# Kernel optimization log

Measured on AMD Instinct MI355X. Metric: run time of the kernel, lower is better.

The kernel has to match this reference:

```python
import jax, jax.numpy as jnp
import numpy as np
from jax import lax

EPS = 1e-5

def _dsconv(x, dw, pw, g, b, m, v, relu):
    # x: [B,C,H,W]; dw: [C,1,3,3] depthwise; pw: [C,C,1,1] pointwise; eval-mode BN
    C = x.shape[1]
    y = lax.conv_general_dilated(x, dw, (1, 1), 'SAME', feature_group_count=C)
    y = lax.conv_general_dilated(y, pw, (1, 1), 'SAME')
    scale = (g * lax.rsqrt(v + EPS))[None, :, None, None]
    y = y * scale + (b - m * g * lax.rsqrt(v + EPS))[None, :, None, None]
    return jnp.maximum(y, 0.0) if relu else y

def _attention(x, wq, bq, wk, bk, wv, bv, gamma):
    b, c, h, w = x.shape
    n = h * w
    xf = x.reshape(b, c, n)                      # [B,C,N]
    q = jnp.einsum('oc,bcn->bon', wq, xf) + bq[None, :, None]   # [B,C/8,N]
    k = jnp.einsum('oc,bcn->bon', wk, xf) + bk[None, :, None]   # [B,C/8,N]
    v = jnp.einsum('oc,bcn->bon', wv, xf) + bv[None, :, None]   # [B,C,N]
    logits = jnp.einsum('bdm,bdn->bmn', q, k)    # q^T k, [B,N,N]
    attn = jax.nn.softmax(logits, axis=2)
    out = jnp.einsum('bcn,bmn->bcm', v, attn).reshape(b, c, h, w)
    return gamma[0] * out + x

def setup_inputs() -> dict:
    key = jax.random.key(0)
    ks = jax.random.split(key, 20)
    B, C, H, W = 64, 256, 32, 32
    C8 = C // 8
    rn = lambda k, s, sc: (jax.random.normal(k, s, dtype=jnp.float32) * sc)
    return {
        'x': rn(ks[0], (B, C, H, W), 1.0),
        'dw1': rn(ks[1], (C, 1, 3, 3), 0.2),
        'pw1': rn(ks[2], (C, C, 1, 1), 0.06),
        'bn1_g': jax.random.uniform(ks[3], (C,), jnp.float32, 0.5, 1.5),
        'bn1_b': rn(ks[4], (C,), 0.1),
        'bn1_m': rn(ks[5], (C,), 0.1),
        'bn1_v': jax.random.uniform(ks[6], (C,), jnp.float32, 0.5, 1.5),
        'dw2': rn(ks[7], (C, 1, 3, 3), 0.2),
        'pw2': rn(ks[8], (C, C, 1, 1), 0.06),
        'bn2_g': jax.random.uniform(ks[9], (C,), jnp.float32, 0.5, 1.5),
        'bn2_b': rn(ks[10], (C,), 0.1),
        'bn2_m': rn(ks[11], (C,), 0.1),
        'bn2_v': jax.random.uniform(ks[12], (C,), jnp.float32, 0.5, 1.5),
        'wq': rn(ks[13], (C8, C), 0.06),
        'bq': rn(ks[14], (C8,), 0.02),
        'wk': rn(ks[15], (C8, C), 0.06),
        'bk': rn(ks[16], (C8,), 0.02),
        'wv': rn(ks[17], (C, C), 0.06),
        'bv': rn(ks[18], (C,), 0.02),
        'gamma': rn(ks[19], (1,), 0.5),
    }

def reference(x, dw1, pw1, bn1_g, bn1_b, bn1_m, bn1_v,
              dw2, pw2, bn2_g, bn2_b, bn2_m, bn2_v,
              wq, bq, wk, bk, wv, bv, gamma):
    out = _dsconv(x, dw1, pw1, bn1_g, bn1_b, bn1_m, bn1_v, relu=True)
    out = _dsconv(out, dw2, pw2, bn2_g, bn2_b, bn2_m, bn2_v, relu=False)
    out = _attention(out + x, wq, bq, wk, bk, wv, bv, gamma)
    return jnp.maximum(out, 0.0)
```

## Files before the change

### kernel.cpp

```cpp
#include <hip/hip_runtime.h>
#include <cstdint>
#include <cstddef>

#define B_ 64
#define C_ 256
#define N_ 1024
#define LOG2E 1.4426950408889634f

typedef short v8s __attribute__((ext_vector_type(8)));
typedef float v4f __attribute__((ext_vector_type(4)));
typedef unsigned int u32;
typedef unsigned short u16;

#define VMCNT(N) asm volatile("s_waitcnt vmcnt(" #N ")" ::: "memory")
#define LGKM0 asm volatile("s_waitcnt lgkmcnt(0)" ::: "memory")
#define SBAR __builtin_amdgcn_s_barrier()
#define SCHEDB __builtin_amdgcn_sched_barrier(0)

__device__ __forceinline__ float bf2f(u16 u) {
  return __uint_as_float(((u32)u) << 16);
}
__device__ __forceinline__ u16 f2bf(float f) {
  u32 x = __float_as_uint(f);
  x += 0x7fffu + ((x >> 16) & 1u);
  return (u16)(x >> 16);
}
__device__ __forceinline__ u32 pack2(float a, float b) {
  return (u32)f2bf(a) | ((u32)f2bf(b) << 16);
}
__device__ __forceinline__ u32 cvtpk(float lo, float hi) {
  u32 r;
  asm("v_cvt_pk_bf16_f32 %0, %1, %2" : "=v"(r) : "v"(lo), "v"(hi));
  return r;
}

typedef __attribute__((address_space(3))) unsigned int lds_as_t;
typedef __attribute__((address_space(1))) const unsigned int glb_as_t;
__device__ __forceinline__ void ld_lds16(const u16* g, u16* l) {
  __builtin_amdgcn_global_load_lds((glb_as_t*)g, (lds_as_t*)l, 16, 0, 0);
}

__global__ __launch_bounds__(256) void prep(
    const float* __restrict__ g1, const float* __restrict__ b1,
    const float* __restrict__ m1, const float* __restrict__ v1,
    const float* __restrict__ g2, const float* __restrict__ b2,
    const float* __restrict__ m2, const float* __restrict__ v2,
    const float* __restrict__ wq, const float* __restrict__ bq,
    const float* __restrict__ wk, const float* __restrict__ bk,
    const float* __restrict__ wv, const float* __restrict__ bv,
    const float* __restrict__ pw1, const float* __restrict__ pw2,
    const float* __restrict__ dw1, const float* __restrict__ dw2,
    float* __restrict__ scale1, float* __restrict__ shift1,
    float* __restrict__ scale2, float* __restrict__ shift2,
    float* __restrict__ dwT1, float* __restrict__ dwT2,
    u16* __restrict__ pw1b, u16* __restrict__ pw2b, u16* __restrict__ wcatb,
    float* __restrict__ bcat) {
  const int gt = blockIdx.x * 256 + threadIdx.x;
  if (gt < 256) {
    float s1 = g1[gt] * rsqrtf(v1[gt] + 1e-5f);
    scale1[gt] = s1;
    shift1[gt] = b1[gt] - m1[gt] * s1;
    float s2 = g2[gt] * rsqrtf(v2[gt] + 1e-5f);
    scale2[gt] = s2;
    shift2[gt] = b2[gt] - m2[gt] * s2;
  }
  if (gt < 320)
    bcat[gt] = (gt < 32) ? bq[gt] * LOG2E
                         : (gt < 64) ? bk[gt - 32] : bv[gt - 64];
  if (gt < 2304) {
    dwT1[(gt % 9) * 256 + gt / 9] = dw1[gt];
    dwT2[(gt % 9) * 256 + gt / 9] = dw2[gt];
  }
  for (int e = gt; e < 65536; e += 16384) {
    pw1b[e] = f2bf(pw1[e]);
    pw2b[e] = f2bf(pw2[e]);
  }
  for (int e = gt; e < 81920; e += 16384) {
    const int o = e >> 8;
    float w = (o < 32) ? wq[e] * LOG2E
                       : (o < 64) ? wk[e - 8192] : wv[e - 16384];
    wcatb[e] = f2bf(w);
  }
}

__global__ __launch_bounds__(256) void transpose_x(const float* __restrict__ x,
                                                   u16* __restrict__ xt) {
  __shared__ float t[64][65];
  const int b = blockIdx.z, c0 = blockIdx.y * 64, n0 = blockIdx.x * 64;
  const float* xp = x + ((size_t)b * C_ + c0) * N_ + n0;
  const int tn = threadIdx.x & 63, tc = threadIdx.x >> 6;
#pragma unroll
  for (int i = 0; i < 16; ++i)
    t[tc + 4 * i][tn] = xp[(size_t)(tc + 4 * i) * N_ + tn];
  __syncthreads();
  u16* op = xt + ((size_t)b * N_ + n0) * C_ + c0;
  const int oc = threadIdx.x & 63, on = threadIdx.x >> 6;
#pragma unroll
  for (int i = 0; i < 16; ++i)
    op[(size_t)(on + 4 * i) * C_ + oc] = f2bf(t[oc][on + 4 * i]);
}

__global__ __launch_bounds__(256) void dw_nhwc(const u16* __restrict__ src,
                                               const float* __restrict__ wT,
                                               u16* __restrict__ dst) {
  __shared__ float wl[9][256];
  const int b = blockIdx.y;
  for (int e = threadIdx.x; e < 2304; e += 256) wl[e >> 8][e & 255] = wT[e];
  __syncthreads();
  const int pl = threadIdx.x >> 5, c0 = (threadIdx.x & 31) * 8;
  const int p = blockIdx.x * 8 + pl;
  const int h = p >> 5, wx = p & 31;
  const u16* sp = src + (size_t)b * N_ * C_;
  float acc[8] = {0.f, 0.f, 0.f, 0.f, 0.f, 0.f, 0.f, 0.f};
#pragma unroll
  for (int dh = -1; dh <= 1; ++dh) {
    const int hh = h + dh;
    if (hh < 0 || hh > 31) continue;
#pragma unroll
    for (int dx = -1; dx <= 1; ++dx) {
      const int ww = wx + dx;
      if (ww < 0 || ww > 31) continue;
      const int k = (dh + 1) * 3 + (dx + 1);
      const uint4 v = *(const uint4*)(sp + (size_t)(hh * 32 + ww) * C_ + c0);
      const u32 vv[4] = {v.x, v.y, v.z, v.w};
#pragma unroll
      for (int j = 0; j < 4; ++j) {
        acc[2 * j] += bf2f((u16)(vv[j] & 0xffffu)) * wl[k][c0 + 2 * j];
        acc[2 * j + 1] += bf2f((u16)(vv[j] >> 16)) * wl[k][c0 + 2 * j + 1];
      }
    }
  }
  uint4 o4;
  o4.x = pack2(acc[0], acc[1]);
  o4.y = pack2(acc[2], acc[3]);
  o4.z = pack2(acc[4], acc[5]);
  o4.w = pack2(acc[6], acc[7]);
  *(uint4*)(dst + ((size_t)b * N_ + p) * C_ + c0) = o4;
}

template <int EPI>
__global__ __launch_bounds__(256, 4) void gemm(
    const u16* __restrict__ X, const u16* __restrict__ W,
    const float* __restrict__ scale, const float* __restrict__ shift,
    const u16* __restrict__ resid, u16* __restrict__ Y, u16* __restrict__ Y2) {
  __shared__ u16 smem[17408];
  u16(*Ys)[136] = (u16(*)[136])smem;
  u16(*YsQ)[68] = (u16(*)[68])smem;

  const int tid = threadIdx.x;
  const int b = blockIdx.z;
  const int n0 = blockIdx.x * 128, o0 = blockIdx.y * 128;
  const int wid = tid >> 6, lane = tid & 63;
  const int wn = wid & 1, wo = wid >> 1;
  const int l15 = lane & 15, l4 = lane >> 4;
  const int r16 = lane >> 2, c16 = (lane & 3) * 8;

  v4f acc[4][4];
#pragma unroll
  for (int i = 0; i < 4; ++i)
#pragma unroll
    for (int j = 0; j < 4; ++j) acc[i][j] = v4f{0.f, 0.f, 0.f, 0.f};

  auto stage = [&](int kidx, int bufsel) {
    const int k0 = (kidx & 7) * 32;
    u16* Xd = smem + bufsel * 8192;
    u16* Wd = Xd + 4096;
#pragma unroll
    for (int g = 0; g < 2; ++g) {
      const int base = wid * 32 + g * 16;
      ld_lds16(X + ((size_t)b * N_ + n0 + base + r16) * C_ + k0 + c16,
               Xd + base * 32);
      int wr = o0 + base + r16;
      if (EPI == 2 && wr > 319) wr = 319;
      ld_lds16(W + (size_t)wr * C_ + k0 + c16, Wd + base * 32);
    }
  };

  stage(0, 0);
  stage(1, 1);

#pragma unroll
  for (int k = 0; k < 8; ++k) {
    const int cur = k & 1;
    if (k < 7) {
      VMCNT(4);
    } else {
      VMCNT(0);
    }
    SCHEDB;
    SBAR;
    const u16(*Xs)[32] = (const u16(*)[32])(smem + cur * 8192);
    const u16(*Ws)[32] = (const u16(*)[32])(smem + cur * 8192 + 4096);
    v8s af[4], bf4[4];
#pragma unroll
    for (int f = 0; f < 4; ++f) {
      if constexpr (EPI != 2) {
        af[f] = *(const v8s*)&Ws[wo * 64 + f * 16 + l15][l4 * 8];
        bf4[f] = *(const v8s*)&Xs[wn * 64 + f * 16 + l15][l4 * 8];
      } else {
        af[f] = *(const v8s*)&Xs[wn * 64 + f * 16 + l15][l4 * 8];
        bf4[f] = *(const v8s*)&Ws[wo * 64 + f * 16 + l15][l4 * 8];
      }
    }
#pragma unroll
    for (int i = 0; i < 4; ++i)
#pragma unroll
      for (int j = 0; j < 4; ++j)
        acc[i][j] = __builtin_amdgcn_mfma_f32_16x16x32_bf16(af[i], bf4[j],
                                                            acc[i][j], 0, 0, 0);
    LGKM0;
    SBAR;
    SCHEDB;
    if (k < 6) stage(k + 2, cur);
  }

  if constexpr (EPI != 2) {
#pragma unroll
    for (int i = 0; i < 4; ++i) {
      const int oL = wo * 64 + i * 16 + l4 * 4;
      const int o = o0 + oL;
      const float4 sc = *(const float4*)&scale[o];
      const float4 sh = *(const float4*)&shift[o];
#pragma unroll
      for (int j = 0; j < 4; ++j) {
        const int nL = wn * 64 + j * 16 + l15;
        float y0 = acc[i][j][0] * sc.x + sh.x;
        float y1 = acc[i][j][1] * sc.y + sh.y;
        float y2 = acc[i][j][2] * sc.z + sh.z;
        float y3 = acc[i][j][3] * sc.w + sh.w;
        if constexpr (EPI == 0) {
          y0 = fmaxf(y0, 0.f);
          y1 = fmaxf(y1, 0.f);
          y2 = fmaxf(y2, 0.f);
          y3 = fmaxf(y3, 0.f);
        } else {
          const uint2 rb =
              *(const uint2*)(resid + ((size_t)b * N_ + n0 + nL) * C_ + o);
          y0 += bf2f((u16)(rb.x & 0xffffu));
          y1 += bf2f((u16)(rb.x >> 16));
          y2 += bf2f((u16)(rb.y & 0xffffu));
          y3 += bf2f((u16)(rb.y >> 16));
        }
        uint2 st;
        st.x = pack2(y0, y1);
        st.y = pack2(y2, y3);
        *(uint2*)&Ys[nL][oL] = st;
      }
    }
    __syncthreads();
#pragma unroll
    for (int s = 0; s < 8; ++s) {
      const int nL = s * 16 + (tid >> 4);
      const int slot = tid & 15;
      const uint4 v = *(const uint4*)&Ys[nL][slot * 8];
      *(uint4*)&Y[((size_t)b * N_ + n0 + nL) * C_ + o0 + slot * 8] = v;
    }
  } else {
    float bj[4];
#pragma unroll
    for (int j = 0; j < 4; ++j) {
      int o = o0 + wo * 64 + j * 16 + l15;
      bj[j] = shift[o > 319 ? 319 : o];
    }
    if (o0 == 0 && wo == 0) {
#pragma unroll
      for (int i = 0; i < 4; ++i) {
        const int nL = wn * 64 + i * 16 + l4 * 4;
#pragma unroll
        for (int j = 0; j < 4; ++j) {
          const int oL = j * 16 + l15;
#pragma unroll
          for (int r = 0; r < 4; ++r)
            YsQ[nL + r][oL] = f2bf(acc[i][j][r] + bj[j]);
        }
      }
    } else {
#pragma unroll
      for (int i = 0; i < 4; ++i) {
        const int nL = wn * 64 + i * 16 + l4 * 4;
#pragma unroll
        for (int j = 0; j < 4; ++j) {
          const int oL = wo * 64 + j * 16 + l15;
          uint2 st;
          st.x = pack2(acc[i][j][0] + bj[j], acc[i][j][1] + bj[j]);
          st.y = pack2(acc[i][j][2] + bj[j], acc[i][j][3] + bj[j]);
          *(uint2*)&Ys[oL][nL] = st;
        }
      }
    }
    __syncthreads();
    if (o0 == 0) {
#pragma unroll
      for (int s = 0; s < 4; ++s) {
        const int e = s * 256 + tid;
        const int row = e >> 3, seg = e & 7;
        const uint4 v = *(const uint4*)&YsQ[row][seg * 8];
        *(uint4*)&Y[((size_t)b * N_ + n0 + row) * 64 + seg * 8] = v;
      }
#pragma unroll
      for (int s = 0; s < 4; ++s) {
        const int e = s * 256 + tid;
        const int oL = 64 + (e >> 4), slot = e & 15;
        const uint4 v = *(const uint4*)&Ys[oL][slot * 8];
        *(uint4*)&Y2[((size_t)b * C_ + oL - 64) * N_ + n0 + slot * 8] = v;
      }
    } else {
#pragma unroll
      for (int s = 0; s < 8; ++s) {
        const int oL = s * 16 + (tid >> 4);
        const int c = o0 + oL - 64;
        if (c < 256) {
          const int slot = tid & 15;
          const uint4 v = *(const uint4*)&Ys[oL][slot * 8];
          *(uint4*)&Y2[((size_t)b * C_ + c) * N_ + n0 + slot * 8] = v;
        }
      }
    }
  }
}

__global__ __launch_bounds__(256, 3) void flash(
    const u16* __restrict__ qk, const u16* __restrict__ vchw,
    const u16* __restrict__ abf, const float* __restrict__ gamma_p,
    float* __restrict__ out) {
  const int b = blockIdx.x;
  const int m0 = blockIdx.y * 64;
  const int tid = threadIdx.x, wid = tid >> 6, lane = tid & 63;
  const int l15 = lane & 15, l4 = lane >> 4;
  const int mw = m0 + wid * 16;
  const int cq = wid * 64;

  __shared__ u16 Vs[256][64];
  __shared__ u16 Pl[2][64][72];
  __shared__ float Sl[64];

  const u16* qkb = qk + (size_t)b * N_ * 64;
  const u16* vb = vchw + (size_t)b * C_ * N_;
  const v8s qf = *(const v8s*)&qkb[(size_t)(mw + l15) * 64 + l4 * 8];

  const int s_row = lane >> 3;
  const int s_j = (lane & 7) ^ (s_row & 7);

  float Mloc = -3e38f;
  {
    v8s kf1[4];
#pragma unroll
    for (int f = 0; f < 4; ++f)
      kf1[f] = *(const v8s*)&qkb[(size_t)(f * 16 + l15) * 64 + 32 + l4 * 8];
    for (int t = 0; t < 16; ++t) {
      v8s kn[4];
      if (t < 15) {
        const int n1 = (t + 1) * 64;
#pragma unroll
        for (int f = 0; f < 4; ++f)
          kn[f] =
              *(const v8s*)&qkb[(size_t)(n1 + f * 16 + l15) * 64 + 32 + l4 * 8];
      }
#pragma unroll
      for (int f = 0; f < 4; ++f) {
        const v4f lt = __builtin_amdgcn_mfma_f32_16x16x32_bf16(
            kf1[f], qf, v4f{0.f, 0.f, 0.f, 0.f}, 0, 0, 0);
        Mloc = fmaxf(Mloc, fmaxf(fmaxf(lt[0], lt[1]), fmaxf(lt[2], lt[3])));
      }
      if (t < 15) {
#pragma unroll
        for (int f = 0; f < 4; ++f) kf1[f] = kn[f];
      }
    }
  }
  Mloc = fmaxf(Mloc, __shfl_xor(Mloc, 16));
  Mloc = fmaxf(Mloc, __shfl_xor(Mloc, 32));
  const float M = Mloc;

  v4f acc[4][4];
#pragma unroll
  for (int mf = 0; mf < 4; ++mf)
#pragma unroll
    for (int j = 0; j < 4; ++j) acc[mf][j] = v4f{0.f, 0.f, 0.f, 0.f};
  float S0 = 0.f, S1 = 0.f, S2 = 0.f, S3 = 0.f;
  v8s kf[4];
#pragma unroll
  for (int f = 0; f < 4; ++f)
    kf[f] = *(const v8s*)&qkb[(size_t)(f * 16 + l15) * 64 + 32 + l4 * 8];
  VMCNT(0);
  SCHEDB;

  {
    v4f lt[4];
#pragma unroll
    for (int f = 0; f < 4; ++f)
      lt[f] = __builtin_amdgcn_mfma_f32_16x16x32_bf16(
          kf[f], qf, v4f{0.f, 0.f, 0.f, 0.f}, 0, 0, 0);
#pragma unroll
    for (int f = 0; f < 4; ++f) {
      const float p0 = exp2f(lt[f][0] - M);
      const float p1 = exp2f(lt[f][1] - M);
      const float p2 = exp2f(lt[f][2] - M);
      const float p3 = exp2f(lt[f][3] - M);
      S0 += p0;
      S1 += p1;
      S2 += p2;
      S3 += p3;
      uint2 pw;
      pw.x = cvtpk(p0, p1);
      pw.y = cvtpk(p2, p3);
      *(uint2*)&Pl[0][wid * 16 + l15][f * 16 + l4 * 4] = pw;
    }
#pragma unroll
    for (int f = 0; f < 4; ++f)
      kf[f] = *(const v8s*)&qkb[(size_t)(64 + f * 16 + l15) * 64 + 32 + l4 * 8];
    SCHEDB;
#pragma unroll
    for (int g = 0; g < 8; ++g) {
      const int base = cq + g * 8;
      ld_lds16(vb + (size_t)(base + s_row) * N_ + s_j * 8, &Vs[base][0]);
    }
    LGKM0;
    SBAR;
  }

  for (int t = 1; t < 16; ++t) {
    const int pb = (t - 1) & 1, cb = t & 1;
    VMCNT(8);
    SCHEDB;
    v4f lt[4];
#pragma unroll
    for (int f = 0; f < 4; ++f)
      lt[f] = __builtin_amdgcn_mfma_f32_16x16x32_bf16(
          kf[f], qf, v4f{0.f, 0.f, 0.f, 0.f}, 0, 0, 0);
    VMCNT(0);
    SCHEDB;
    __builtin_amdgcn_s_setprio(1);
#pragma unroll
    for (int ks = 0; ks < 2; ++ks) {
      v8s pa[4];
#pragma unroll
      for (int mf = 0; mf < 4; ++mf)
        pa[mf] = *(const v8s*)&Pl[pb][mf * 16 + l15][ks * 32 + l4 * 8];
#pragma unroll
      for (int j = 0; j < 4; ++j) {
        const int col = 8 * (((ks * 4) + l4) ^ (l15 & 7));
        const v8s vf = *(const v8s*)&Vs[cq + j * 16 + l15][col];
#pragma unroll
        for (int mf = 0; mf < 4; ++mf)
          acc[mf][j] = __builtin_amdgcn_mfma_f32_16x16x32_bf16(
              pa[mf], vf, acc[mf][j], 0, 0, 0);
      }
    }
    __builtin_amdgcn_s_setprio(0);
#pragma unroll
    for (int f = 0; f < 4; ++f) {
      const float p0 = exp2f(lt[f][0] - M);
      const float p1 = exp2f(lt[f][1] - M);
      const float p2 = exp2f(lt[f][2] - M);
      const float p3 = exp2f(lt[f][3] - M);
      S0 += p0;
      S1 += p1;
      S2 += p2;
      S3 += p3;
      uint2 pw;
      pw.x = cvtpk(p0, p1);
      pw.y = cvtpk(p2, p3);
      *(uint2*)&Pl[cb][wid * 16 + l15][f * 16 + l4 * 4] = pw;
    }
    {
      const int n1 = ((t + 1) & 15) * 64;
#pragma unroll
      for (int f = 0; f < 4; ++f)
        kf[f] =
            *(const v8s*)&qkb[(size_t)(n1 + f * 16 + l15) * 64 + 32 + l4 * 8];
    }
    SCHEDB;
    {
      const int n1 = t * 64;
#pragma unroll
      for (int g = 0; g < 8; ++g) {
        const int base = cq + g * 8;
        ld_lds16(vb + (size_t)(base + s_row) * N_ + n1 + s_j * 8, &Vs[base][0]);
      }
    }
    LGKM0;
    SBAR;
  }

  VMCNT(0);
  SCHEDB;
  __builtin_amdgcn_s_setprio(1);
#pragma unroll
  for (int ks = 0; ks < 2; ++ks) {
    v8s pa[4];
#pragma unroll
    for (int mf = 0; mf < 4; ++mf)
      pa[mf] = *(const v8s*)&Pl[1][mf * 16 + l15][ks * 32 + l4 * 8];
#pragma unroll
    for (int j = 0; j < 4; ++j) {
      const int col = 8 * (((ks * 4) + l4) ^ (l15 & 7));
      const v8s vf = *(const v8s*)&Vs[cq + j * 16 + l15][col];
#pragma unroll
      for (int mf = 0; mf < 4; ++mf)
        acc[mf][j] = __builtin_amdgcn_mfma_f32_16x16x32_bf16(
            pa[mf], vf, acc[mf][j], 0, 0, 0);
    }
  }
  __builtin_amdgcn_s_setprio(0);

  float S = (S0 + S1) + (S2 + S3);
  S += __shfl_xor(S, 16);
  S += __shfl_xor(S, 32);
  if (lane < 16) Sl[wid * 16 + lane] = 1.f / S;
  __syncthreads();

  const float gma = gamma_p[0];
  float invv[4][4];
#pragma unroll
  for (int mf = 0; mf < 4; ++mf)
#pragma unroll
    for (int r = 0; r < 4; ++r) invv[mf][r] = Sl[mf * 16 + l4 * 4 + r];

#pragma unroll
  for (int mf = 0; mf < 4; ++mf) {
    const int mb = m0 + mf * 16 + l4 * 4;
#pragma unroll
    for (int j = 0; j < 4; ++j) {
      const int c = cq + j * 16 + l15;
      float4 y;
      float* yp = (float*)&y;
#pragma unroll
      for (int r = 0; r < 4; ++r) {
        const float av = bf2f(abf[((size_t)b * N_ + mb + r) * C_ + c]);
        yp[r] = fmaxf(gma * acc[mf][j][r] * invv[mf][r] + av, 0.f);
      }
      *(float4*)&out[((size_t)b * C_ + c) * N_ + mb] = y;
    }
  }
}

extern "C" void kernel_launch(void* const* d_in, const int* in_sizes, int n_in,
                              void* d_out, int out_size, void* d_ws,
                              size_t ws_size, hipStream_t stream) {
  const float* x = (const float*)d_in[0];
  const float* dw1 = (const float*)d_in[1];
  const float* pw1 = (const float*)d_in[2];
  const float* bn1g = (const float*)d_in[3];
  const float* bn1b = (const float*)d_in[4];
  const float* bn1m = (const float*)d_in[5];
  const float* bn1v = (const float*)d_in[6];
  const float* dw2 = (const float*)d_in[7];
  const float* pw2 = (const float*)d_in[8];
  const float* bn2g = (const float*)d_in[9];
  const float* bn2b = (const float*)d_in[10];
  const float* bn2m = (const float*)d_in[11];
  const float* bn2v = (const float*)d_in[12];
  const float* wq = (const float*)d_in[13];
  const float* bq = (const float*)d_in[14];
  const float* wk = (const float*)d_in[15];
  const float* bk = (const float*)d_in[16];
  const float* wv = (const float*)d_in[17];
  const float* bv = (const float*)d_in[18];
  const float* gamma = (const float*)d_in[19];
  float* out = (float*)d_out;

  char* ws = (char*)d_ws;
  size_t off = 0;
  auto alloc = [&](size_t bytes) {
    void* p = ws + off;
    off += (bytes + 255) & ~(size_t)255;
    return p;
  };
  const size_t NE = (size_t)B_ * N_ * C_;

  u16* bufA = (u16*)alloc(NE * 2);
  u16* bufB = (u16*)alloc(NE * 2);
  u16* bufC = (u16*)alloc(NE * 2);
  u16* abf = (u16*)alloc(NE * 2);
  float* scale1 = (float*)alloc(256 * 4);
  float* shift1 = (float*)alloc(256 * 4);
  float* scale2 = (float*)alloc(256 * 4);
  float* shift2 = (float*)alloc(256 * 4);
  float* dwT1 = (float*)alloc(2304 * 4);
  float* dwT2 = (float*)alloc(2304 * 4);
  u16* pw1b = (u16*)alloc(65536 * 2);
  u16* pw2b = (u16*)alloc(65536 * 2);
  u16* wcatb = (u16*)alloc(81920 * 2);
  float* bcat = (float*)alloc(384 * 4);

  u16* xt = bufA;
  u16* t1 = bufB;
  u16* y1 = bufC;
  u16* t2 = bufB;
  u16* qkbuf = bufC;
  u16* vchw = bufA;

  prep<<<64, 256, 0, stream>>>(bn1g, bn1b, bn1m, bn1v, bn2g, bn2b, bn2m, bn2v,
                               wq, bq, wk, bk, wv, bv, pw1, pw2, dw1, dw2,
                               scale1, shift1, scale2, shift2, dwT1, dwT2,
                               pw1b, pw2b, wcatb, bcat);
  transpose_x<<<dim3(16, 4, B_), 256, 0, stream>>>(x, xt);
  dw_nhwc<<<dim3(128, B_), 256, 0, stream>>>(xt, dwT1, t1);
  gemm<0><<<dim3(8, 2, B_), 256, 0, stream>>>(t1, pw1b, scale1, shift1,
                                              nullptr, y1, nullptr);
  dw_nhwc<<<dim3(128, B_), 256, 0, stream>>>(y1, dwT2, t2);
  gemm<1><<<dim3(8, 2, B_), 256, 0, stream>>>(t2, pw2b, scale2, shift2, xt,
                                              abf, nullptr);
  gemm<2><<<dim3(8, 3, B_), 256, 0, stream>>>(abf, wcatb, nullptr, bcat,
                                              nullptr, qkbuf, vchw);
  flash<<<dim3(64, 16), 256, 0, stream>>>(qkbuf, vchw, abf, gamma, out);
}
```

Measured before the change: 252.0 us.

## Use online softmax in flash kernel and stage residual tile through LDS

Drops the separate pre-pass that computed the row max over all 1024 keys with a full extra QK^T sweep. Instead each tile updates a running max, rescales the accumulators by a per-row factor passed through shared memory, and carries a running sum. The epilogue also loads the bf16 residual tile into LDS with coalesced 16-byte loads, replacing the scattered 2-byte global reads, and reuses the V/P buffer space for it. The cost is extra rescale multiplies, shuffles and an exp per tile, plus one more barrier.

```diff
diff --git a/kernel.cpp b/kernel.cpp
--- a/kernel.cpp
+++ b/kernel.cpp
@@ -330,9 +330,12 @@
   const int mw = m0 + wid * 16;
   const int cq = wid * 64;
 
-  __shared__ u16 Vs[256][64];
-  __shared__ u16 Pl[2][64][72];
+  __shared__ u16 pool[25600];
+  __shared__ float fscL[2][64];
   __shared__ float Sl[64];
+  u16(*Vs)[64] = (u16(*)[64])pool;
+  u16(*Pl)[64][72] = (u16(*)[64][72])(pool + 16384);
+  u16* AB = pool;
 
   const u16* qkb = qk + (size_t)b * N_ * 64;
   const u16* vb = vchw + (size_t)b * C_ * N_;
@@ -341,43 +344,13 @@
   const int s_row = lane >> 3;
   const int s_j = (lane & 7) ^ (s_row & 7);
 
-  float Mloc = -3e38f;
-  {
-    v8s kf1[4];
-#pragma unroll
-    for (int f = 0; f < 4; ++f)
-      kf1[f] = *(const v8s*)&qkb[(size_t)(f * 16 + l15) * 64 + 32 + l4 * 8];
-    for (int t = 0; t < 16; ++t) {
-      v8s kn[4];
-      if (t < 15) {
-        const int n1 = (t + 1) * 64;
-#pragma unroll
-        for (int f = 0; f < 4; ++f)
-          kn[f] =
-              *(const v8s*)&qkb[(size_t)(n1 + f * 16 + l15) * 64 + 32 + l4 * 8];
-      }
-#pragma unroll
-      for (int f = 0; f < 4; ++f) {
-        const v4f lt = __builtin_amdgcn_mfma_f32_16x16x32_bf16(
-            kf1[f], qf, v4f{0.f, 0.f, 0.f, 0.f}, 0, 0, 0);
-        Mloc = fmaxf(Mloc, fmaxf(fmaxf(lt[0], lt[1]), fmaxf(lt[2], lt[3])));
-      }
-      if (t < 15) {
-#pragma unroll
-        for (int f = 0; f < 4; ++f) kf1[f] = kn[f];
-      }
-    }
-  }
-  Mloc = fmaxf(Mloc, __shfl_xor(Mloc, 16));
-  Mloc = fmaxf(Mloc, __shfl_xor(Mloc, 32));
-  const float M = Mloc;
-
   v4f acc[4][4];
 #pragma unroll
   for (int mf = 0; mf < 4; ++mf)
 #pragma unroll
     for (int j = 0; j < 4; ++j) acc[mf][j] = v4f{0.f, 0.f, 0.f, 0.f};
-  float S0 = 0.f, S1 = 0.f, S2 = 0.f, S3 = 0.f;
+  float M = -3e38f, S = 0.f;
+
   v8s kf[4];
 #pragma unroll
   for (int f = 0; f < 4; ++f)
@@ -391,21 +364,31 @@
     for (int f = 0; f < 4; ++f)
       lt[f] = __builtin_amdgcn_mfma_f32_16x16x32_bf16(
           kf[f], qf, v4f{0.f, 0.f, 0.f, 0.f}, 0, 0, 0);
+    float pmax = -3e38f;
+#pragma unroll
+    for (int f = 0; f < 4; ++f)
+#pragma unroll
+      for (int r = 0; r < 4; ++r) pmax = fmaxf(pmax, lt[f][r]);
+    pmax = fmaxf(pmax, __shfl_xor(pmax, 16));
+    pmax = fmaxf(pmax, __shfl_xor(pmax, 32));
+    const float Mn = fmaxf(M, pmax);
+    const float fsc = exp2f(M - Mn);
+    float sum = 0.f;
 #pragma unroll
     for (int f = 0; f < 4; ++f) {
-      const float p0 = exp2f(lt[f][0] - M);
-      const float p1 = exp2f(lt[f][1] - M);
-      const float p2 = exp2f(lt[f][2] - M);
-      const float p3 = exp2f(lt[f][3] - M);
-      S0 += p0;
-      S1 += p1;
-      S2 += p2;
-      S3 += p3;
+      const float p0 = exp2f(lt[f][0] - Mn);
+      const float p1 = exp2f(lt[f][1] - Mn);
+      const float p2 = exp2f(lt[f][2] - Mn);
+      const float p3 = exp2f(lt[f][3] - Mn);
+      sum += (p0 + p1) + (p2 + p3);
       uint2 pw;
       pw.x = cvtpk(p0, p1);
       pw.y = cvtpk(p2, p3);
       *(uint2*)&Pl[0][wid * 16 + l15][f * 16 + l4 * 4] = pw;
     }
+    S = S * fsc + sum;
+    M = Mn;
+    if (l4 == 0) fscL[0][wid * 16 + l15] = fsc;
 #pragma unroll
     for (int f = 0; f < 4; ++f)
       kf[f] = *(const v8s*)&qkb[(size_t)(64 + f * 16 + l15) * 64 + 32 + l4 * 8];
@@ -428,6 +411,18 @@
     for (int f = 0; f < 4; ++f)
       lt[f] = __builtin_amdgcn_mfma_f32_16x16x32_bf16(
           kf[f], qf, v4f{0.f, 0.f, 0.f, 0.f}, 0, 0, 0);
+    {
+      v4f fr[4];
+#pragma unroll
+      for (int mf = 0; mf < 4; ++mf)
+        fr[mf] = *(const v4f*)&fscL[pb][mf * 16 + l4 * 4];
+#pragma unroll
+      for (int mf = 0; mf < 4; ++mf)
+#pragma unroll
+        for (int j = 0; j < 4; ++j)
+#pragma unroll
+          for (int r = 0; r < 4; ++r) acc[mf][j][r] *= fr[mf][r];
+    }
     VMCNT(0);
     SCHEDB;
     __builtin_amdgcn_s_setprio(1);
@@ -448,20 +443,32 @@
       }
     }
     __builtin_amdgcn_s_setprio(0);
-#pragma unroll
-    for (int f = 0; f < 4; ++f) {
-      const float p0 = exp2f(lt[f][0] - M);
-      const float p1 = exp2f(lt[f][1] - M);
-      const float p2 = exp2f(lt[f][2] - M);
-      const float p3 = exp2f(lt[f][3] - M);
-      S0 += p0;
-      S1 += p1;
-      S2 += p2;
-      S3 += p3;
-      uint2 pw;
-      pw.x = cvtpk(p0, p1);
-      pw.y = cvtpk(p2, p3);
-      *(uint2*)&Pl[cb][wid * 16 + l15][f * 16 + l4 * 4] = pw;
+    {
+      float pmax = -3e38f;
+#pragma unroll
+      for (int f = 0; f < 4; ++f)
+#pragma unroll
+        for (int r = 0; r < 4; ++r) pmax = fmaxf(pmax, lt[f][r]);
+      pmax = fmaxf(pmax, __shfl_xor(pmax, 16));
+      pmax = fmaxf(pmax, __shfl_xor(pmax, 32));
+      const float Mn = fmaxf(M, pmax);
+      const float fsc = exp2f(M - Mn);
+      float sum = 0.f;
+#pragma unroll
+      for (int f = 0; f < 4; ++f) {
+        const float p0 = exp2f(lt[f][0] - Mn);
+        const float p1 = exp2f(lt[f][1] - Mn);
+        const float p2 = exp2f(lt[f][2] - Mn);
+        const float p3 = exp2f(lt[f][3] - Mn);
+        sum += (p0 + p1) + (p2 + p3);
+        uint2 pw;
+        pw.x = cvtpk(p0, p1);
+        pw.y = cvtpk(p2, p3);
+        *(uint2*)&Pl[cb][wid * 16 + l15][f * 16 + l4 * 4] = pw;
+      }
+      S = S * fsc + sum;
+      M = Mn;
+      if (l4 == 0) fscL[cb][wid * 16 + l15] = fsc;
     }
     {
       const int n1 = ((t + 1) & 15) * 64;
@@ -485,6 +492,18 @@
 
   VMCNT(0);
   SCHEDB;
+  {
+    v4f fr[4];
+#pragma unroll
+    for (int mf = 0; mf < 4; ++mf)
+      fr[mf] = *(const v4f*)&fscL[1][mf * 16 + l4 * 4];
+#pragma unroll
+    for (int mf = 0; mf < 4; ++mf)
+#pragma unroll
+      for (int j = 0; j < 4; ++j)
+#pragma unroll
+        for (int r = 0; r < 4; ++r) acc[mf][j][r] *= fr[mf][r];
+  }
   __builtin_amdgcn_s_setprio(1);
 #pragma unroll
   for (int ks = 0; ks < 2; ++ks) {
@@ -504,19 +523,27 @@
   }
   __builtin_amdgcn_s_setprio(0);
 
-  float S = (S0 + S1) + (S2 + S3);
   S += __shfl_xor(S, 16);
   S += __shfl_xor(S, 32);
   if (lane < 16) Sl[wid * 16 + lane] = 1.f / S;
   __syncthreads();
 
+#pragma unroll
+  for (int s = 0; s < 8; ++s) {
+    const int e = s * 256 + tid;
+    const int row = e >> 5, col = (e & 31) * 8;
+    const uint4 v =
+        *(const uint4*)(abf + ((size_t)b * N_ + m0 + row) * C_ + col);
+    *(uint4*)&AB[row * 264 + col] = v;
+  }
+  float invv[4][4];
+#pragma unroll
+  for (int mf = 0; mf < 4; ++mf)
+#pragma unroll
+    for (int r = 0; r < 4; ++r) invv[mf][r] = Sl[mf * 16 + l4 * 4 + r];
+  __syncthreads();
+
   const float gma = gamma_p[0];
-  float invv[4][4];
-#pragma unroll
-  for (int mf = 0; mf < 4; ++mf)
-#pragma unroll
-    for (int r = 0; r < 4; ++r) invv[mf][r] = Sl[mf * 16 + l4 * 4 + r];
-
 #pragma unroll
   for (int mf = 0; mf < 4; ++mf) {
     const int mb = m0 + mf * 16 + l4 * 4;
@@ -527,7 +554,7 @@
       float* yp = (float*)&y;
 #pragma unroll
       for (int r = 0; r < 4; ++r) {
-        const float av = bf2f(abf[((size_t)b * N_ + mb + r) * C_ + c]);
+        const float av = bf2f(AB[(mf * 16 + l4 * 4 + r) * 264 + c]);
         yp[r] = fmaxf(gma * acc[mf][j][r] * invv[mf][r] + av, 0.f);
       }
       *(float4*)&out[((size_t)b * C_ + c) * N_ + mb] = y;
```

New measurement: 231.0 us. 1.09x faster.
